# Kernel tuning notes

Measured on AMD Instinct MI355X. Metric: run time of the kernel, lower is better.

The kernel has to match this reference:

```python
import jax, jax.numpy as jnp
import numpy as np

V, D, B, L = 100000, 64, 4096, 200

def setup_inputs() -> dict:
    key = jax.random.key(0)
    ks = jax.random.split(key, 10)
    s = 0.05  # keep activations in a sane range for sigmoid
    return {
        "item_ids": jax.random.randint(ks[0], (B,), 0, V),
        "history": jax.random.randint(ks[1], (B, L), 0, V),
        "hist_len": jax.random.randint(ks[2], (B,), 1, L + 1),
        "emb_table": jax.random.normal(ks[3], (V, D), jnp.float32) * s,
        "aW1": jax.random.normal(ks[4], (3 * D, D), jnp.float32) * s,
        "ab1": jnp.zeros((D,), jnp.float32),
        "aW2": jax.random.normal(ks[5], (D, 1), jnp.float32) * s,
        "ab2": jnp.zeros((1,), jnp.float32),
        "fW1": jax.random.normal(ks[6], (3 * D, 128), jnp.float32) * s,
        "fb1": jnp.zeros((128,), jnp.float32),
        "fW2": jax.random.normal(ks[7], (128, 64), jnp.float32) * s,
        "fb2": jnp.zeros((64,), jnp.float32),
        "fW3": jax.random.normal(ks[8], (64, 1), jnp.float32) * s,
        "fb3": jnp.zeros((1,), jnp.float32),
    }

def reference(item_ids, history, hist_len, emb_table, aW1, ab1, aW2, ab2,
              fW1, fb1, fW2, fb2, fW3, fb3):
    target = emb_table[item_ids]                      # [B, D]
    hist = emb_table[history]                         # [B, L, D]
    # original pads short histories with zero rows -> zero the padded tail
    mask = (jnp.arange(hist.shape[1])[None, :] < hist_len[:, None]).astype(hist.dtype)
    hist = hist * mask[..., None]
    tgt = jnp.broadcast_to(target[:, None, :], hist.shape)     # [B, L, D]
    # attention_fc takes 3*D features: (hist, target, hist*target)
    feat = jnp.concatenate([hist, tgt, hist * tgt], axis=-1)   # [B, L, 3D]
    h = jax.nn.relu(feat @ aW1 + ab1)                 # [B, L, D]
    scores = (h @ aW2 + ab2)[..., 0]                  # [B, L]
    # faithful to original: softmax over full padded length (no length mask)
    w = jax.nn.softmax(scores, axis=1)
    pooled = jnp.einsum('bl,bld->bd', w, hist)        # [B, D]
    comb = jnp.concatenate([target, pooled, pooled - target], axis=-1)  # [B, 3D]
    z = jax.nn.relu(comb @ fW1 + fb1)
    z = jax.nn.relu(z @ fW2 + fb2)
    return jax.nn.sigmoid(z @ fW3 + fb3)              # [B, 1]
```

## Files before the change

kernel.cpp:

```cpp
#include <hip/hip_runtime.h>
#include <hip/hip_bf16.h>

#define NV 100000
#define ND 64
#define NB 4096
#define NL 200
#define MT 13

typedef __bf16 bf16_t;
typedef __bf16 bf16x8 __attribute__((ext_vector_type(8)));
typedef float f32x4 __attribute__((ext_vector_type(4)));

#define TB_ELEMS ((long)NV * ND)

__global__ __launch_bounds__(256)
void cvt_kernel(const float* __restrict__ emb, bf16_t* __restrict__ tb)
{
    long i = ((long)blockIdx.x * 256 + threadIdx.x) * 8;
    if (i < TB_ELEMS) {
        f32x4 a0 = *(const f32x4*)(emb + i);
        f32x4 a1 = *(const f32x4*)(emb + i + 4);
        bf16x8 o;
#pragma unroll
        for (int j = 0; j < 4; ++j) { o[j] = (bf16_t)a0[j]; o[j + 4] = (bf16_t)a1[j]; }
        *(bf16x8*)(tb + i) = o;
    }
}

__global__ __launch_bounds__(256, 4)
void din_kernel1(const int* __restrict__ item_ids,
                 const int* __restrict__ history,
                 const int* __restrict__ hist_len,
                 const float* __restrict__ emb,
                 const bf16_t* __restrict__ tb,
                 const float* __restrict__ aW1,
                 const float* __restrict__ ab1,
                 const float* __restrict__ aW2,
                 const float* __restrict__ fW1, const float* __restrict__ fb1,
                 const float* __restrict__ fW2, const float* __restrict__ fb2,
                 const float* __restrict__ fW3, const float* __restrict__ fb3,
                 float* __restrict__ out)
{
    __shared__ __align__(16) bf16_t histA[208 * 64];
    __shared__ __align__(16) bf16_t wbT[64 * 64];
    __shared__ float tgt[64];
    __shared__ float cb[64];
    __shared__ __align__(16) float scores[208];
    __shared__ float wts[208];
    __shared__ float pp[4 * 64];
    __shared__ float red[8];
    __shared__ float pooled[64];

    float* mlp_pp = (float*)wbT;
    float* z1     = (float*)wbT + 1024;
    float* z2     = (float*)wbT + 1152;
    float* comb_l = scores;

    const int b   = blockIdx.x;
    const int tid = threadIdx.x;
    const int len = hist_len[b];

    if (tid < 64) tgt[tid] = emb[(long)item_ids[b] * ND + tid];

    {
        const int p  = tid & 1;
        const int l0 = tid >> 1;
        const int l1 = l0 + 128;
        const bf16x8 z = (bf16x8)(bf16_t)0.f;
        bf16x8 v00 = z, v01 = z, v02 = z, v03 = z;
        bf16x8 v10 = z, v11 = z, v12 = z, v13 = z;
        if (l0 < len) {
            const bf16_t* s = tb + (long)history[(long)b * NL + l0] * ND + p * 32;
            v00 = *(const bf16x8*)(s);
            v01 = *(const bf16x8*)(s + 8);
            v02 = *(const bf16x8*)(s + 16);
            v03 = *(const bf16x8*)(s + 24);
        }
        if (l1 < len) {
            const bf16_t* s = tb + (long)history[(long)b * NL + l1] * ND + p * 32;
            v10 = *(const bf16x8*)(s);
            v11 = *(const bf16x8*)(s + 8);
            v12 = *(const bf16x8*)(s + 16);
            v13 = *(const bf16x8*)(s + 24);
        }
        {
            bf16_t* d = &histA[l0 * 64];
            const int S = (l0 & 7) << 3;
            *(bf16x8*)&d[(p * 32 +  0) ^ S] = v00;
            *(bf16x8*)&d[(p * 32 +  8) ^ S] = v01;
            *(bf16x8*)&d[(p * 32 + 16) ^ S] = v02;
            *(bf16x8*)&d[(p * 32 + 24) ^ S] = v03;
        }
        if (l1 < 208) {
            bf16_t* d = &histA[l1 * 64];
            const int S = (l1 & 7) << 3;
            *(bf16x8*)&d[(p * 32 +  0) ^ S] = v10;
            *(bf16x8*)&d[(p * 32 +  8) ^ S] = v11;
            *(bf16x8*)&d[(p * 32 + 16) ^ S] = v12;
            *(bf16x8*)&d[(p * 32 + 24) ^ S] = v13;
        }
    }

    {
        const int n    = tid & 63;
        const int kp   = tid >> 6;
        const long trow = (long)item_ids[b] * ND;
        float csum = 0.f;
        bf16x8 w0, w1;
#pragma unroll
        for (int i = 0; i < 16; ++i) {
            int k = kp * 16 + i;
            float tk = emb[trow + k];
            float w  = aW1[k * 64 + n] + tk * aW1[(128 + k) * 64 + n];
            if (i < 8) w0[i] = (bf16_t)w; else w1[i - 8] = (bf16_t)w;
            csum += tk * aW1[(64 + k) * 64 + n];
        }
        const int S = (n & 7) << 3;
        *(bf16x8*)&wbT[n * 64 + ((kp * 16    ) ^ S)] = w0;
        *(bf16x8*)&wbT[n * 64 + ((kp * 16 + 8) ^ S)] = w1;
        pp[kp * 64 + n] = csum;
    }
    __syncthreads();
    if (tid < 64) cb[tid] = ab1[tid] + pp[tid] + pp[64 + tid] + pp[128 + tid] + pp[192 + tid];
    __syncthreads();

    {
        const int wave = tid >> 6;
        const int lane = tid & 63;
        const int col  = lane & 15;
        const int quad = lane >> 4;

        bf16x8 bfrag[4][2];
#pragma unroll
        for (int nt = 0; nt < 4; ++nt) {
            const int n = nt * 16 + col;
            const int S = (n & 7) << 3;
#pragma unroll
            for (int kb = 0; kb < 2; ++kb)
                bfrag[nt][kb] = *(const bf16x8*)&wbT[n * 64 + ((kb * 32 + quad * 8) ^ S)];
        }
        float cvals[4], a2vals[4];
#pragma unroll
        for (int nt = 0; nt < 4; ++nt) {
            cvals[nt]  = cb[nt * 16 + col];
            a2vals[nt] = aW2[nt * 16 + col];
        }

        for (int mt = wave; mt < MT; mt += 4) {
            const int row = mt * 16 + col;
            const int S   = (row & 7) << 3;
            const bf16_t* base = &histA[row * 64];
            bf16x8 af0 = *(const bf16x8*)&base[(     quad * 8) ^ S];
            bf16x8 af1 = *(const bf16x8*)&base[(32 + quad * 8) ^ S];
            float sc[4] = {0.f, 0.f, 0.f, 0.f};
#pragma unroll
            for (int nt = 0; nt < 4; ++nt) {
                f32x4 acc = {0.f, 0.f, 0.f, 0.f};
                acc = __builtin_amdgcn_mfma_f32_16x16x32_bf16(af0, bfrag[nt][0], acc, 0, 0, 0);
                acc = __builtin_amdgcn_mfma_f32_16x16x32_bf16(af1, bfrag[nt][1], acc, 0, 0, 0);
#pragma unroll
                for (int i = 0; i < 4; ++i) {
                    float h = acc[i] + cvals[nt];
                    h = h > 0.f ? h : 0.f;
                    sc[i] += h * a2vals[nt];
                }
            }
            for (int off = 1; off < 16; off <<= 1)
#pragma unroll
                for (int i = 0; i < 4; ++i)
                    sc[i] += __shfl_xor(sc[i], off, 64);
            if (col == 0) {
                f32x4 outv = {sc[0], sc[1], sc[2], sc[3]};
                *(f32x4*)&scores[mt * 16 + quad * 4] = outv;
            }
        }
    }
    __syncthreads();

    {
        float s = (tid < NL) ? scores[tid] : -1e30f;
        float m = s;
        for (int off = 32; off > 0; off >>= 1) m = fmaxf(m, __shfl_xor(m, off, 64));
        if ((tid & 63) == 0) red[tid >> 6] = m;
        __syncthreads();
        m = fmaxf(fmaxf(red[0], red[1]), fmaxf(red[2], red[3]));
        float e = (tid < NL) ? __expf(s - m) : 0.f;
        float ssum = e;
        for (int off = 32; off > 0; off >>= 1) ssum += __shfl_xor(ssum, off, 64);
        if ((tid & 63) == 0) red[4 + (tid >> 6)] = ssum;
        __syncthreads();
        float tot = red[4] + red[5] + red[6] + red[7];
        if (tid < NL) wts[tid] = e / tot;
    }
    __syncthreads();

    {
        const int wave = tid >> 6, lane = tid & 63;
        float acc = 0.f;
        for (int i = 0; i < 50; ++i) {
            int l = wave * 50 + i;
            float wl = wts[l];
            acc += wl * (float)histA[l * 64 + (lane ^ ((l & 7) << 3))];
        }
        pp[wave * 64 + lane] = acc;
    }
    __syncthreads();
    if (tid < 64) pooled[tid] = pp[tid] + pp[64 + tid] + pp[128 + tid] + pp[192 + tid];
    __syncthreads();

    if (tid < 192) {
        float v;
        if (tid < 64)       v = tgt[tid];
        else if (tid < 128) v = pooled[tid - 64];
        else                v = pooled[tid - 128] - tgt[tid - 128];
        comb_l[tid] = v;
    }
    __syncthreads();

    {
        const int c = tid & 31;
        const int g = tid >> 5;
        f32x4 acc = {0.f, 0.f, 0.f, 0.f};
#pragma unroll
        for (int ii = 0; ii < 24; ++ii) {
            int i = g * 24 + ii;
            float cm = comb_l[i];
            f32x4 w = *(const f32x4*)(fW1 + (long)i * 128 + c * 4);
#pragma unroll
            for (int jj = 0; jj < 4; ++jj) acc[jj] += cm * w[jj];
        }
        *(f32x4*)&mlp_pp[g * 128 + c * 4] = acc;
    }
    __syncthreads();
    if (tid < 128) {
        float s = fb1[tid];
#pragma unroll
        for (int g = 0; g < 8; ++g) s += mlp_pp[g * 128 + tid];
        z1[tid] = fmaxf(s, 0.f);
    }
    __syncthreads();

    {
        const int c = tid & 15;
        const int g = tid >> 4;
        f32x4 acc = {0.f, 0.f, 0.f, 0.f};
#pragma unroll
        for (int ii = 0; ii < 8; ++ii) {
            int i = g * 8 + ii;
            float zv = z1[i];
            f32x4 w = *(const f32x4*)(fW2 + (long)i * 64 + c * 4);
#pragma unroll
            for (int jj = 0; jj < 4; ++jj) acc[jj] += zv * w[jj];
        }
        *(f32x4*)&mlp_pp[g * 64 + c * 4] = acc;
    }
    __syncthreads();
    if (tid < 64) {
        float s = fb2[tid];
#pragma unroll
        for (int g = 0; g < 16; ++g) s += mlp_pp[g * 64 + tid];
        z2[tid] = fmaxf(s, 0.f);
    }
    __syncthreads();

    if (tid < 64) {
        float s = z2[tid] * fW3[tid];
        for (int off = 32; off > 0; off >>= 1) s += __shfl_xor(s, off, 64);
        if (tid == 0) out[b] = 1.f / (1.f + __expf(-(s + fb3[0])));
    }
}

extern "C" void kernel_launch(void* const* d_in, const int* in_sizes, int n_in,
                              void* d_out, int out_size, void* d_ws, size_t ws_size,
                              hipStream_t stream) {
    const int*   item_ids = (const int*)d_in[0];
    const int*   history  = (const int*)d_in[1];
    const int*   hist_len = (const int*)d_in[2];
    const float* emb      = (const float*)d_in[3];
    const float* aW1      = (const float*)d_in[4];
    const float* ab1      = (const float*)d_in[5];
    const float* aW2      = (const float*)d_in[6];
    const float* fW1      = (const float*)d_in[8];
    const float* fb1      = (const float*)d_in[9];
    const float* fW2      = (const float*)d_in[10];
    const float* fb2      = (const float*)d_in[11];
    const float* fW3      = (const float*)d_in[12];
    const float* fb3      = (const float*)d_in[13];

    bf16_t* tb = (bf16_t*)d_ws;

    cvt_kernel<<<(int)(TB_ELEMS / 8 / 256 + 1), 256, 0, stream>>>(emb, tb);
    din_kernel1<<<NB, 256, 0, stream>>>(item_ids, history, hist_len, emb, tb,
                                        aW1, ab1, aW2,
                                        fW1, fb1, fW2, fb2, fW3, fb3,
                                        (float*)d_out);
}
```

Before: 149.8 us.

## Process two batch rows per 512-thread block and use bf16 MLP weights

Each block now handles two samples with 512 threads. This shares the aW1 loads used to fold the target into the attention weights, and shares the fW1/fW2 weight reads across both samples in the final MLP. The MLP weights are converted to bf16 in the existing conversion kernel, which halves their read traffic. Softmax normalisation is deferred into the pooling step, which removes a barrier. Shared memory per block roughly doubles, so occupancy may drop, and the bf16 MLP weights add rounding error.

```diff
diff --git a/kernel.cpp b/kernel.cpp
--- a/kernel.cpp
+++ b/kernel.cpp
@@ -12,22 +12,31 @@
 typedef float f32x4 __attribute__((ext_vector_type(4)));
 
 #define TB_ELEMS ((long)NV * ND)
+#define FW1_ELEMS (192 * 128)
+#define FW2_ELEMS (128 * 64)
+#define CVT_TOTAL (TB_ELEMS + FW1_ELEMS + FW2_ELEMS)
 
 __global__ __launch_bounds__(256)
-void cvt_kernel(const float* __restrict__ emb, bf16_t* __restrict__ tb)
+void cvt_kernel(const float* __restrict__ emb,
+                const float* __restrict__ fW1,
+                const float* __restrict__ fW2,
+                bf16_t* __restrict__ tb)
 {
     long i = ((long)blockIdx.x * 256 + threadIdx.x) * 8;
-    if (i < TB_ELEMS) {
-        f32x4 a0 = *(const f32x4*)(emb + i);
-        f32x4 a1 = *(const f32x4*)(emb + i + 4);
-        bf16x8 o;
-#pragma unroll
-        for (int j = 0; j < 4; ++j) { o[j] = (bf16_t)a0[j]; o[j + 4] = (bf16_t)a1[j]; }
-        *(bf16x8*)(tb + i) = o;
-    }
+    if (i >= CVT_TOTAL) return;
+    const float* src;
+    if (i < TB_ELEMS)                  src = emb + i;
+    else if (i < TB_ELEMS + FW1_ELEMS) src = fW1 + (i - TB_ELEMS);
+    else                               src = fW2 + (i - TB_ELEMS - FW1_ELEMS);
+    f32x4 a0 = *(const f32x4*)(src);
+    f32x4 a1 = *(const f32x4*)(src + 4);
+    bf16x8 o;
+#pragma unroll
+    for (int j = 0; j < 4; ++j) { o[j] = (bf16_t)a0[j]; o[j + 4] = (bf16_t)a1[j]; }
+    *(bf16x8*)(tb + i) = o;
 }
 
-__global__ __launch_bounds__(256, 4)
+__global__ __launch_bounds__(512, 4)
 void din_kernel1(const int* __restrict__ item_ids,
                  const int* __restrict__ history,
                  const int* __restrict__ hist_len,
@@ -36,97 +45,112 @@
                  const float* __restrict__ aW1,
                  const float* __restrict__ ab1,
                  const float* __restrict__ aW2,
-                 const float* __restrict__ fW1, const float* __restrict__ fb1,
-                 const float* __restrict__ fW2, const float* __restrict__ fb2,
+                 const bf16_t* __restrict__ fW1b, const float* __restrict__ fb1,
+                 const bf16_t* __restrict__ fW2b, const float* __restrict__ fb2,
                  const float* __restrict__ fW3, const float* __restrict__ fb3,
                  float* __restrict__ out)
 {
-    __shared__ __align__(16) bf16_t histA[208 * 64];
-    __shared__ __align__(16) bf16_t wbT[64 * 64];
-    __shared__ float tgt[64];
-    __shared__ float cb[64];
-    __shared__ __align__(16) float scores[208];
-    __shared__ float wts[208];
-    __shared__ float pp[4 * 64];
-    __shared__ float red[8];
-    __shared__ float pooled[64];
-
-    float* mlp_pp = (float*)wbT;
-    float* z1     = (float*)wbT + 1024;
-    float* z2     = (float*)wbT + 1152;
-    float* comb_l = scores;
-
-    const int b   = blockIdx.x;
+    __shared__ __align__(16) bf16_t histA[2][208 * 64];
+    __shared__ __align__(16) bf16_t wbT[2][64 * 64];
+    __shared__ float tgt[2][64];
+    __shared__ __align__(16) float scores[2][208];
+    __shared__ float wts[2][208];
+    __shared__ float pp2[2][512];
+    __shared__ float red[2][8];
+
+    float* pp7 = (float*)histA;
+    float* z1  = (float*)histA + 8192;
+    float* z2  = (float*)histA + 8448;
+
+    const int b0  = blockIdx.x * 2;
     const int tid = threadIdx.x;
-    const int len = hist_len[b];
-
-    if (tid < 64) tgt[tid] = emb[(long)item_ids[b] * ND + tid];
-
-    {
-        const int p  = tid & 1;
-        const int l0 = tid >> 1;
-        const int l1 = l0 + 128;
+    const int len0 = hist_len[b0];
+    const int len1 = hist_len[b0 + 1];
+
+    if (tid < 128) {
+        int bx = tid >> 6, d = tid & 63;
+        tgt[bx][d] = emb[(long)item_ids[b0 + bx] * ND + d];
+    }
+
+    {
+        const int p = tid & 1;
+        const int s = tid >> 1;
+        const int bxA = (s >= 208);
+        const int lA  = s - bxA * 208;
+        const int lB  = s + 48;
+        const int lenA = bxA ? len1 : len0;
+        const bool vB = (s < 160);
         const bf16x8 z = (bf16x8)(bf16_t)0.f;
-        bf16x8 v00 = z, v01 = z, v02 = z, v03 = z;
-        bf16x8 v10 = z, v11 = z, v12 = z, v13 = z;
-        if (l0 < len) {
-            const bf16_t* s = tb + (long)history[(long)b * NL + l0] * ND + p * 32;
-            v00 = *(const bf16x8*)(s);
-            v01 = *(const bf16x8*)(s + 8);
-            v02 = *(const bf16x8*)(s + 16);
-            v03 = *(const bf16x8*)(s + 24);
-        }
-        if (l1 < len) {
-            const bf16_t* s = tb + (long)history[(long)b * NL + l1] * ND + p * 32;
-            v10 = *(const bf16x8*)(s);
-            v11 = *(const bf16x8*)(s + 8);
-            v12 = *(const bf16x8*)(s + 16);
-            v13 = *(const bf16x8*)(s + 24);
+        bf16x8 a0 = z, a1 = z, a2 = z, a3 = z;
+        bf16x8 c0 = z, c1 = z, c2 = z, c3 = z;
+        if (lA < lenA) {
+            const bf16_t* src = tb + (long)history[(long)(b0 + bxA) * NL + lA] * ND + p * 32;
+            a0 = *(const bf16x8*)(src);
+            a1 = *(const bf16x8*)(src + 8);
+            a2 = *(const bf16x8*)(src + 16);
+            a3 = *(const bf16x8*)(src + 24);
+        }
+        if (vB && lB < len1) {
+            const bf16_t* src = tb + (long)history[(long)(b0 + 1) * NL + lB] * ND + p * 32;
+            c0 = *(const bf16x8*)(src);
+            c1 = *(const bf16x8*)(src + 8);
+            c2 = *(const bf16x8*)(src + 16);
+            c3 = *(const bf16x8*)(src + 24);
         }
         {
-            bf16_t* d = &histA[l0 * 64];
-            const int S = (l0 & 7) << 3;
-            *(bf16x8*)&d[(p * 32 +  0) ^ S] = v00;
-            *(bf16x8*)&d[(p * 32 +  8) ^ S] = v01;
-            *(bf16x8*)&d[(p * 32 + 16) ^ S] = v02;
-            *(bf16x8*)&d[(p * 32 + 24) ^ S] = v03;
-        }
-        if (l1 < 208) {
-            bf16_t* d = &histA[l1 * 64];
-            const int S = (l1 & 7) << 3;
-            *(bf16x8*)&d[(p * 32 +  0) ^ S] = v10;
-            *(bf16x8*)&d[(p * 32 +  8) ^ S] = v11;
-            *(bf16x8*)&d[(p * 32 + 16) ^ S] = v12;
-            *(bf16x8*)&d[(p * 32 + 24) ^ S] = v13;
-        }
-    }
-
-    {
-        const int n    = tid & 63;
-        const int kp   = tid >> 6;
-        const long trow = (long)item_ids[b] * ND;
-        float csum = 0.f;
-        bf16x8 w0, w1;
-#pragma unroll
-        for (int i = 0; i < 16; ++i) {
-            int k = kp * 16 + i;
-            float tk = emb[trow + k];
-            float w  = aW1[k * 64 + n] + tk * aW1[(128 + k) * 64 + n];
-            if (i < 8) w0[i] = (bf16_t)w; else w1[i - 8] = (bf16_t)w;
-            csum += tk * aW1[(64 + k) * 64 + n];
+            bf16_t* d = &histA[bxA][lA * 64];
+            const int S = (lA & 7) << 3;
+            *(bf16x8*)&d[(p * 32 +  0) ^ S] = a0;
+            *(bf16x8*)&d[(p * 32 +  8) ^ S] = a1;
+            *(bf16x8*)&d[(p * 32 + 16) ^ S] = a2;
+            *(bf16x8*)&d[(p * 32 + 24) ^ S] = a3;
+        }
+        if (vB) {
+            bf16_t* d = &histA[1][lB * 64];
+            const int S = (lB & 7) << 3;
+            *(bf16x8*)&d[(p * 32 +  0) ^ S] = c0;
+            *(bf16x8*)&d[(p * 32 +  8) ^ S] = c1;
+            *(bf16x8*)&d[(p * 32 + 16) ^ S] = c2;
+            *(bf16x8*)&d[(p * 32 + 24) ^ S] = c3;
+        }
+    }
+
+    {
+        const int n  = tid & 63;
+        const int kp = tid >> 6;
+        const long t0 = (long)item_ids[b0] * ND;
+        const long t1 = (long)item_ids[b0 + 1] * ND;
+        f32x4 tk0a = *(const f32x4*)(emb + t0 + kp * 8);
+        f32x4 tk0b = *(const f32x4*)(emb + t0 + kp * 8 + 4);
+        f32x4 tk1a = *(const f32x4*)(emb + t1 + kp * 8);
+        f32x4 tk1b = *(const f32x4*)(emb + t1 + kp * 8 + 4);
+        float cs0 = 0.f, cs1 = 0.f;
+        bf16x8 w0v, w1v;
+#pragma unroll
+        for (int i = 0; i < 8; ++i) {
+            int k = kp * 8 + i;
+            float tk0 = (i < 4) ? tk0a[i] : tk0b[i - 4];
+            float tk1 = (i < 4) ? tk1a[i] : tk1b[i - 4];
+            float ah = aW1[k * 64 + n];
+            float am = aW1[(64 + k) * 64 + n];
+            float ap = aW1[(128 + k) * 64 + n];
+            w0v[i] = (bf16_t)(ah + tk0 * ap);
+            w1v[i] = (bf16_t)(ah + tk1 * ap);
+            cs0 += tk0 * am;
+            cs1 += tk1 * am;
         }
         const int S = (n & 7) << 3;
-        *(bf16x8*)&wbT[n * 64 + ((kp * 16    ) ^ S)] = w0;
-        *(bf16x8*)&wbT[n * 64 + ((kp * 16 + 8) ^ S)] = w1;
-        pp[kp * 64 + n] = csum;
-    }
-    __syncthreads();
-    if (tid < 64) cb[tid] = ab1[tid] + pp[tid] + pp[64 + tid] + pp[128 + tid] + pp[192 + tid];
+        *(bf16x8*)&wbT[0][n * 64 + ((kp * 8) ^ S)] = w0v;
+        *(bf16x8*)&wbT[1][n * 64 + ((kp * 8) ^ S)] = w1v;
+        pp2[0][kp * 64 + n] = cs0;
+        pp2[1][kp * 64 + n] = cs1;
+    }
     __syncthreads();
 
     {
         const int wave = tid >> 6;
         const int lane = tid & 63;
+        const int bx   = wave & 1;
         const int col  = lane & 15;
         const int quad = lane >> 4;
 
@@ -137,19 +161,23 @@
             const int S = (n & 7) << 3;
 #pragma unroll
             for (int kb = 0; kb < 2; ++kb)
-                bfrag[nt][kb] = *(const bf16x8*)&wbT[n * 64 + ((kb * 32 + quad * 8) ^ S)];
+                bfrag[nt][kb] = *(const bf16x8*)&wbT[bx][n * 64 + ((kb * 32 + quad * 8) ^ S)];
         }
         float cvals[4], a2vals[4];
 #pragma unroll
         for (int nt = 0; nt < 4; ++nt) {
-            cvals[nt]  = cb[nt * 16 + col];
-            a2vals[nt] = aW2[nt * 16 + col];
-        }
-
-        for (int mt = wave; mt < MT; mt += 4) {
+            const int n = nt * 16 + col;
+            float s = ab1[n];
+#pragma unroll
+            for (int kp = 0; kp < 8; ++kp) s += pp2[bx][kp * 64 + n];
+            cvals[nt]  = s;
+            a2vals[nt] = aW2[n];
+        }
+
+        for (int mt = (wave >> 1); mt < MT; mt += 4) {
             const int row = mt * 16 + col;
             const int S   = (row & 7) << 3;
-            const bf16_t* base = &histA[row * 64];
+            const bf16_t* base = &histA[bx][row * 64];
             bf16x8 af0 = *(const bf16x8*)&base[(     quad * 8) ^ S];
             bf16x8 af1 = *(const bf16x8*)&base[(32 + quad * 8) ^ S];
             float sc[4] = {0.f, 0.f, 0.f, 0.f};
@@ -171,102 +199,125 @@
                     sc[i] += __shfl_xor(sc[i], off, 64);
             if (col == 0) {
                 f32x4 outv = {sc[0], sc[1], sc[2], sc[3]};
-                *(f32x4*)&scores[mt * 16 + quad * 4] = outv;
-            }
-        }
-    }
-    __syncthreads();
-
-    {
-        float s = (tid < NL) ? scores[tid] : -1e30f;
+                *(f32x4*)&scores[bx][mt * 16 + quad * 4] = outv;
+            }
+        }
+    }
+    __syncthreads();
+
+    {
+        const int bx = tid >> 8, t = tid & 255;
+        float s = (t < NL) ? scores[bx][t] : -1e30f;
         float m = s;
         for (int off = 32; off > 0; off >>= 1) m = fmaxf(m, __shfl_xor(m, off, 64));
-        if ((tid & 63) == 0) red[tid >> 6] = m;
+        if ((t & 63) == 0) red[bx][t >> 6] = m;
         __syncthreads();
-        m = fmaxf(fmaxf(red[0], red[1]), fmaxf(red[2], red[3]));
-        float e = (tid < NL) ? __expf(s - m) : 0.f;
-        float ssum = e;
-        for (int off = 32; off > 0; off >>= 1) ssum += __shfl_xor(ssum, off, 64);
-        if ((tid & 63) == 0) red[4 + (tid >> 6)] = ssum;
+        m = fmaxf(fmaxf(red[bx][0], red[bx][1]), fmaxf(red[bx][2], red[bx][3]));
+        float e = (t < NL) ? __expf(s - m) : 0.f;
+        if (t < NL) wts[bx][t] = e;
+        float ss = e;
+        for (int off = 32; off > 0; off >>= 1) ss += __shfl_xor(ss, off, 64);
+        if ((t & 63) == 0) red[bx][4 + (t >> 6)] = ss;
         __syncthreads();
-        float tot = red[4] + red[5] + red[6] + red[7];
-        if (tid < NL) wts[tid] = e / tot;
-    }
-    __syncthreads();
+    }
 
     {
         const int wave = tid >> 6, lane = tid & 63;
+        const int bx = wave >> 2, q = wave & 3;
+        const float rtot = 1.f / (red[bx][4] + red[bx][5] + red[bx][6] + red[bx][7]);
         float acc = 0.f;
         for (int i = 0; i < 50; ++i) {
-            int l = wave * 50 + i;
-            float wl = wts[l];
-            acc += wl * (float)histA[l * 64 + (lane ^ ((l & 7) << 3))];
-        }
-        pp[wave * 64 + lane] = acc;
-    }
-    __syncthreads();
-    if (tid < 64) pooled[tid] = pp[tid] + pp[64 + tid] + pp[128 + tid] + pp[192 + tid];
-    __syncthreads();
-
-    if (tid < 192) {
-        float v;
-        if (tid < 64)       v = tgt[tid];
-        else if (tid < 128) v = pooled[tid - 64];
-        else                v = pooled[tid - 128] - tgt[tid - 128];
-        comb_l[tid] = v;
-    }
-    __syncthreads();
-
-    {
-        const int c = tid & 31;
-        const int g = tid >> 5;
-        f32x4 acc = {0.f, 0.f, 0.f, 0.f};
-#pragma unroll
-        for (int ii = 0; ii < 24; ++ii) {
-            int i = g * 24 + ii;
-            float cm = comb_l[i];
-            f32x4 w = *(const f32x4*)(fW1 + (long)i * 128 + c * 4);
-#pragma unroll
-            for (int jj = 0; jj < 4; ++jj) acc[jj] += cm * w[jj];
-        }
-        *(f32x4*)&mlp_pp[g * 128 + c * 4] = acc;
+            int l = q * 50 + i;
+            acc += wts[bx][l] * (float)histA[bx][l * 64 + (lane ^ ((l & 7) << 3))];
+        }
+        pp2[bx][q * 64 + lane] = acc * rtot;
+    }
+    __syncthreads();
+
+    {
+        const int bx = tid >> 8, t = tid & 255;
+        if (t < 192) {
+            const int d = t & 63;
+            float v;
+            if (t < 64) v = tgt[bx][d];
+            else {
+                float pl = pp2[bx][d] + pp2[bx][64 + d] + pp2[bx][128 + d] + pp2[bx][192 + d];
+                v = (t < 128) ? pl : pl - tgt[bx][d];
+            }
+            scores[bx][t] = v;
+        }
+    }
+    __syncthreads();
+
+    {
+        const int cg = tid & 15;
+        const int g  = tid >> 4;
+        f32x4 a00 = {0,0,0,0}, a01 = {0,0,0,0};
+        f32x4 a10 = {0,0,0,0}, a11 = {0,0,0,0};
+#pragma unroll
+        for (int ii = 0; ii < 6; ++ii) {
+            int i = g * 6 + ii;
+            bf16x8 wv = *(const bf16x8*)&fW1b[i * 128 + cg * 8];
+            float c0 = scores[0][i], c1 = scores[1][i];
+#pragma unroll
+            for (int jj = 0; jj < 4; ++jj) {
+                float wA = (float)wv[jj], wB = (float)wv[4 + jj];
+                a00[jj] += c0 * wA;  a01[jj] += c0 * wB;
+                a10[jj] += c1 * wA;  a11[jj] += c1 * wB;
+            }
+        }
+        *(f32x4*)&pp7[g * 256 +       cg * 8    ] = a00;
+        *(f32x4*)&pp7[g * 256 +       cg * 8 + 4] = a01;
+        *(f32x4*)&pp7[g * 256 + 128 + cg * 8    ] = a10;
+        *(f32x4*)&pp7[g * 256 + 128 + cg * 8 + 4] = a11;
+    }
+    __syncthreads();
+    if (tid < 256) {
+        const int bx = tid >> 7, j = tid & 127;
+        float s = fb1[j];
+#pragma unroll
+        for (int g = 0; g < 32; ++g) s += pp7[g * 256 + bx * 128 + j];
+        z1[bx * 128 + j] = fmaxf(s, 0.f);
+    }
+    __syncthreads();
+
+    {
+        const int cg = tid & 7;
+        const int g  = tid >> 3;
+        f32x4 a00 = {0,0,0,0}, a01 = {0,0,0,0};
+        f32x4 a10 = {0,0,0,0}, a11 = {0,0,0,0};
+#pragma unroll
+        for (int ii = 0; ii < 2; ++ii) {
+            int i = g * 2 + ii;
+            bf16x8 wv = *(const bf16x8*)&fW2b[i * 64 + cg * 8];
+            float v0 = z1[i], v1 = z1[128 + i];
+#pragma unroll
+            for (int jj = 0; jj < 4; ++jj) {
+                float wA = (float)wv[jj], wB = (float)wv[4 + jj];
+                a00[jj] += v0 * wA;  a01[jj] += v0 * wB;
+                a10[jj] += v1 * wA;  a11[jj] += v1 * wB;
+            }
+        }
+        *(f32x4*)&pp7[g * 128 +      cg * 8    ] = a00;
+        *(f32x4*)&pp7[g * 128 +      cg * 8 + 4] = a01;
+        *(f32x4*)&pp7[g * 128 + 64 + cg * 8    ] = a10;
+        *(f32x4*)&pp7[g * 128 + 64 + cg * 8 + 4] = a11;
     }
     __syncthreads();
     if (tid < 128) {
-        float s = fb1[tid];
-#pragma unroll
-        for (int g = 0; g < 8; ++g) s += mlp_pp[g * 128 + tid];
-        z1[tid] = fmaxf(s, 0.f);
-    }
-    __syncthreads();
-
-    {
-        const int c = tid & 15;
-        const int g = tid >> 4;
-        f32x4 acc = {0.f, 0.f, 0.f, 0.f};
-#pragma unroll
-        for (int ii = 0; ii < 8; ++ii) {
-            int i = g * 8 + ii;
-            float zv = z1[i];
-            f32x4 w = *(const f32x4*)(fW2 + (long)i * 64 + c * 4);
-#pragma unroll
-            for (int jj = 0; jj < 4; ++jj) acc[jj] += zv * w[jj];
-        }
-        *(f32x4*)&mlp_pp[g * 64 + c * 4] = acc;
-    }
-    __syncthreads();
-    if (tid < 64) {
-        float s = fb2[tid];
-#pragma unroll
-        for (int g = 0; g < 16; ++g) s += mlp_pp[g * 64 + tid];
-        z2[tid] = fmaxf(s, 0.f);
-    }
-    __syncthreads();
-
-    if (tid < 64) {
-        float s = z2[tid] * fW3[tid];
+        const int bx = tid >> 6, j = tid & 63;
+        float s = fb2[j];
+#pragma unroll
+        for (int g = 0; g < 64; ++g) s += pp7[g * 128 + bx * 64 + j];
+        z2[bx * 64 + j] = fmaxf(s, 0.f);
+    }
+    __syncthreads();
+
+    if (tid < 128) {
+        const int bx = tid >> 6, j = tid & 63;
+        float s = z2[bx * 64 + j] * fW3[j];
         for (int off = 32; off > 0; off >>= 1) s += __shfl_xor(s, off, 64);
-        if (tid == 0) out[b] = 1.f / (1.f + __expf(-(s + fb3[0])));
+        if (j == 0) out[b0 + bx] = 1.f / (1.f + __expf(-(s + fb3[0])));
     }
 }
 
@@ -287,11 +338,13 @@
     const float* fW3      = (const float*)d_in[12];
     const float* fb3      = (const float*)d_in[13];
 
-    bf16_t* tb = (bf16_t*)d_ws;
-
-    cvt_kernel<<<(int)(TB_ELEMS / 8 / 256 + 1), 256, 0, stream>>>(emb, tb);
-    din_kernel1<<<NB, 256, 0, stream>>>(item_ids, history, hist_len, emb, tb,
-                                        aW1, ab1, aW2,
-                                        fW1, fb1, fW2, fb2, fW3, fb3,
-                                        (float*)d_out);
+    bf16_t* tb   = (bf16_t*)d_ws;
+    bf16_t* fW1b = tb + TB_ELEMS;
+    bf16_t* fW2b = fW1b + FW1_ELEMS;
+
+    cvt_kernel<<<(int)((CVT_TOTAL / 8 + 255) / 256), 256, 0, stream>>>(emb, fW1, fW2, tb);
+    din_kernel1<<<NB / 2, 512, 0, stream>>>(item_ids, history, hist_len, emb, tb,
+                                            aW1, ab1, aW2,
+                                            fW1b, fb1, fW2b, fb2, fW3, fb3,
+                                            (float*)d_out);
 }
```

Result: no change. 149.1 us (-0.5%).
